# Performance work log

Hardware: AMD Instinct MI355X
Metric: run time of the kernel (lower is better)

Reference implementation:

```python
import jax, jax.numpy as jnp
import numpy as np

HIDDEN = 768
VOCAB = 32000
HS1 = 128


def setup_inputs() -> dict:
    key = jax.random.key(0)
    k_tk, k_hs, k_w1, k_b1, k_w2, k_b2 = jax.random.split(key, 6)
    B, S = 16, 4096
    tk = jax.random.randint(k_tk, (B, S), 0, VOCAB, dtype=jnp.int64)
    hs0 = jax.random.normal(k_hs, (B, S, HIDDEN), dtype=jnp.float32)
    # lin1: in_features = VOCAB + HIDDEN, out = HS1.  Stored as [in, out]
    # (transpose of torch's [out, in]); rows [0:VOCAB] multiply the one-hot,
    # rows [VOCAB:] multiply hs0, matching cat([one_hot, hs0], -1).
    bound1 = 1.0 / np.sqrt(VOCAB + HIDDEN)
    W1 = jax.random.uniform(k_w1, (VOCAB + HIDDEN, HS1), jnp.float32, -bound1, bound1)
    b1 = jax.random.uniform(k_b1, (HS1,), jnp.float32, -bound1, bound1)
    bound2 = 1.0 / np.sqrt(HS1)
    W2 = jax.random.uniform(k_w2, (HS1, 1), jnp.float32, -bound2, bound2)
    b2 = jax.random.uniform(k_b2, (1,), jnp.float32, -bound2, bound2)
    return {"tk": tk, "hs0": hs0, "W1": W1, "b1": b1, "W2": W2, "b2": b2}


def reference(tk, hs0, W1, b1, W2, b2):
    # one_hot(tk) @ W1[:VOCAB] is exactly a row gather (entries are 0/1),
    # so compute it as a gather fused with the hs0 projection.
    tok_part = W1[:VOCAB][tk]                      # [B, S, HS1] gather
    hs_part = jnp.einsum("bsh,hk->bsk", hs0, W1[VOCAB:])  # [B, S, HS1]
    h = jax.nn.relu(tok_part + hs_part + b1)       # [B, S, HS1]
    out = jnp.einsum("bsk,ko->bso", h, W2) + b2    # [B, S, 1]
    return out.squeeze(-1)                         # [B, S]
```

## Files before the change

### kernel.cpp

```cpp
#include <hip/hip_runtime.h>

#define HIDDEN 768
#define VOCAB  32000
#define HS1    128
#define KSTEPS (HIDDEN / 32)

typedef __attribute__((ext_vector_type(8))) short bf16x8;
typedef __attribute__((ext_vector_type(4))) float f32x4;

__device__ __forceinline__ unsigned short f2bf(float f) {
    union { float f; unsigned u; } x; x.f = f;
    unsigned r = x.u + 0x7fffu + ((x.u >> 16) & 1u);
    return (unsigned short)(r >> 16);
}

__global__ void pack_b_kernel(const float* __restrict__ W1,
                              unsigned short* __restrict__ Bp) {
    int idx  = blockIdx.x * 256 + threadIdx.x;
    int j    = idx & 7;
    int lane = (idx >> 3) & 63;
    int nt   = (idx >> 9) & 7;
    int ks   = idx >> 12;
    int k = ks * 32 + (lane >> 4) * 8 + j;
    int n = nt * 16 + (lane & 15);
    float v = W1[(size_t)(VOCAB + k) * HS1 + n];
    Bp[idx] = f2bf(v);
}

__launch_bounds__(256, 2)
__global__ void classifier_kernel(const int* __restrict__ tk,
                                  const float* __restrict__ hs0,
                                  const float* __restrict__ W1,
                                  const float* __restrict__ b1,
                                  const float* __restrict__ W2,
                                  const float* __restrict__ b2,
                                  const unsigned short* __restrict__ Bp,
                                  float* __restrict__ out) {
    const int lane = threadIdx.x & 63;
    const int wave = threadIdx.x >> 6;
    const int quad = lane >> 4;
    const int col  = lane & 15;
    const int row0 = (blockIdx.x * 4 + wave) * 32;

    const float* a0 = hs0 + (size_t)(row0 + col) * HIDDEN + quad * 8;
    const float* a1 = a0 + (size_t)16 * HIDDEN;
    const unsigned short* bp = Bp + lane * 8;

    f32x4 acc[2][8];
#pragma unroll
    for (int mt = 0; mt < 2; ++mt)
#pragma unroll
        for (int nt = 0; nt < 8; ++nt)
            acc[mt][nt] = (f32x4){0.f, 0.f, 0.f, 0.f};

    struct Frag {
        f32x4 a0l, a0h, a1l, a1h;
        bf16x8 b[8];
    };

    auto load_frag = [&](int ks) {
        Frag f;
        const float* pa0 = a0 + ks * 32;
        const float* pa1 = a1 + ks * 32;
        f.a0l = *(const f32x4*)(pa0);
        f.a0h = *(const f32x4*)(pa0 + 4);
        f.a1l = *(const f32x4*)(pa1);
        f.a1h = *(const f32x4*)(pa1 + 4);
        const unsigned short* pb = bp + ks * 4096;
#pragma unroll
        for (int nt = 0; nt < 8; ++nt)
            f.b[nt] = *(const bf16x8*)(pb + nt * 512);
        return f;
    };

    auto cvt8 = [&](f32x4 lo, f32x4 hi) {
        bf16x8 r;
        r[0] = (short)f2bf(lo[0]); r[1] = (short)f2bf(lo[1]);
        r[2] = (short)f2bf(lo[2]); r[3] = (short)f2bf(lo[3]);
        r[4] = (short)f2bf(hi[0]); r[5] = (short)f2bf(hi[1]);
        r[6] = (short)f2bf(hi[2]); r[7] = (short)f2bf(hi[3]);
        return r;
    };

    auto compute = [&](const Frag& f) {
        bf16x8 af0 = cvt8(f.a0l, f.a0h);
        bf16x8 af1 = cvt8(f.a1l, f.a1h);
#pragma unroll
        for (int nt = 0; nt < 8; ++nt) {
            acc[0][nt] = __builtin_amdgcn_mfma_f32_16x16x32_bf16(af0, f.b[nt], acc[0][nt], 0, 0, 0);
            acc[1][nt] = __builtin_amdgcn_mfma_f32_16x16x32_bf16(af1, f.b[nt], acc[1][nt], 0, 0, 0);
        }
    };

    Frag fa = load_frag(0);
    Frag fb = load_frag(1);
#pragma unroll 1
    for (int ks = 2; ks < KSTEPS; ks += 2) {
        compute(fa);
        fa = load_frag(ks);
        compute(fb);
        fb = load_frag(ks + 1);
    }
    compute(fa);
    compute(fb);

    const float bb2 = b2[0];
    float b1v[8], w2v[8];
#pragma unroll
    for (int nt = 0; nt < 8; ++nt) {
        b1v[nt] = b1[nt * 16 + col];
        w2v[nt] = W2[nt * 16 + col];
    }
#pragma unroll
    for (int mt = 0; mt < 2; ++mt) {
#pragma unroll
        for (int reg = 0; reg < 4; ++reg) {
            int r = row0 + mt * 16 + quad * 4 + reg;
            int token = tk[r];
            const float* wrow = W1 + (size_t)token * HS1;
            float p = 0.f;
#pragma unroll
            for (int nt = 0; nt < 8; ++nt) {
                float v = acc[mt][nt][reg] + wrow[nt * 16 + col] + b1v[nt];
                v = fmaxf(v, 0.f);
                p = fmaf(v, w2v[nt], p);
            }
            p += __shfl_xor(p, 1);
            p += __shfl_xor(p, 2);
            p += __shfl_xor(p, 4);
            p += __shfl_xor(p, 8);
            if (col == 0) out[r] = p + bb2;
        }
    }
}

extern "C" void kernel_launch(void* const* d_in, const int* in_sizes, int n_in,
                              void* d_out, int out_size, void* d_ws, size_t ws_size,
                              hipStream_t stream) {
    const int*   tk  = (const int*)d_in[0];
    const float* hs0 = (const float*)d_in[1];
    const float* W1  = (const float*)d_in[2];
    const float* b1  = (const float*)d_in[3];
    const float* W2  = (const float*)d_in[4];
    const float* b2  = (const float*)d_in[5];
    float* out = (float*)d_out;
    unsigned short* Bp = (unsigned short*)d_ws;

    pack_b_kernel<<<(HIDDEN * HS1) / 256, 256, 0, stream>>>(W1, Bp);

    int n_tokens = in_sizes[0];
    int grid = n_tokens / 128;
    classifier_kernel<<<grid, 256, 0, stream>>>(tk, hs0, W1, b1, W2, b2, Bp, out);
}
```

Measured before the change: 311.8 us.

## Deepen hs0 prefetch to three stages, use nontemporal loads, hoist token reads

The main K loop now keeps three fragments in flight instead of two, so more of the streaming hs0 memory latency is hidden behind MFMA work. The hs0 loads become nontemporal so the streamed activations do not evict the packed weights from cache. Token ids are read before the GEMM loop so the gather addresses are ready at the epilogue. The extra fragment raises register use, which under launch_bounds(256,2) may cause spills or lower occupancy.

```diff
diff --git a/kernel.cpp b/kernel.cpp
--- a/kernel.cpp
+++ b/kernel.cpp
@@ -42,9 +42,16 @@
     const int col  = lane & 15;
     const int row0 = (blockIdx.x * 4 + wave) * 32;
 
-    const float* a0 = hs0 + (size_t)(row0 + col) * HIDDEN + quad * 8;
-    const float* a1 = a0 + (size_t)16 * HIDDEN;
-    const unsigned short* bp = Bp + lane * 8;
+    const float* pa0 = hs0 + (size_t)(row0 + col) * HIDDEN + quad * 8;
+    const float* pa1 = pa0 + (size_t)16 * HIDDEN;
+    const unsigned short* pb0 = Bp + lane * 8;
+
+    int toks[8];
+#pragma unroll
+    for (int mt = 0; mt < 2; ++mt)
+#pragma unroll
+        for (int reg = 0; reg < 4; ++reg)
+            toks[mt * 4 + reg] = tk[row0 + mt * 16 + quad * 4 + reg];
 
     f32x4 acc[2][8];
 #pragma unroll
@@ -60,16 +67,19 @@
 
     auto load_frag = [&](int ks) {
         Frag f;
-        const float* pa0 = a0 + ks * 32;
-        const float* pa1 = a1 + ks * 32;
-        f.a0l = *(const f32x4*)(pa0);
-        f.a0h = *(const f32x4*)(pa0 + 4);
-        f.a1l = *(const f32x4*)(pa1);
-        f.a1h = *(const f32x4*)(pa1 + 4);
-        const unsigned short* pb = bp + ks * 4096;
+        const f32x4* x0 = (const f32x4*)(pa0 + ks * 32);
+        const f32x4* x1 = (const f32x4*)(pa1 + ks * 32);
+        f.a0l = __builtin_nontemporal_load(x0);
+        f.a0h = __builtin_nontemporal_load(x0 + 1);
+        f.a1l = __builtin_nontemporal_load(x1);
+        f.a1h = __builtin_nontemporal_load(x1 + 1);
+        const unsigned short* pb  = pb0 + ks * 4096;
+        const unsigned short* pb2 = pb + 2048;
 #pragma unroll
-        for (int nt = 0; nt < 8; ++nt)
-            f.b[nt] = *(const bf16x8*)(pb + nt * 512);
+        for (int nt = 0; nt < 4; ++nt) {
+            f.b[nt]     = *(const bf16x8*)(pb  + nt * 512);
+            f.b[nt + 4] = *(const bf16x8*)(pb2 + nt * 512);
+        }
         return f;
     };
 
@@ -92,17 +102,18 @@
         }
     };
 
-    Frag fa = load_frag(0);
-    Frag fb = load_frag(1);
+    Frag f0 = load_frag(0);
+    Frag f1 = load_frag(1);
+    Frag f2 = load_frag(2);
 #pragma unroll 1
-    for (int ks = 2; ks < KSTEPS; ks += 2) {
-        compute(fa);
-        fa = load_frag(ks);
-        compute(fb);
-        fb = load_frag(ks + 1);
+    for (int ks = 3; ks < KSTEPS; ks += 3) {
+        compute(f0); f0 = load_frag(ks);
+        compute(f1); f1 = load_frag(ks + 1);
+        compute(f2); f2 = load_frag(ks + 2);
     }
-    compute(fa);
-    compute(fb);
+    compute(f0);
+    compute(f1);
+    compute(f2);
 
     const float bb2 = b2[0];
     float b1v[8], w2v[8];
@@ -116,8 +127,7 @@
 #pragma unroll
         for (int reg = 0; reg < 4; ++reg) {
             int r = row0 + mt * 16 + quad * 4 + reg;
-            int token = tk[r];
-            const float* wrow = W1 + (size_t)token * HS1;
+            const float* wrow = W1 + (size_t)toks[mt * 4 + reg] * HS1;
             float p = 0.f;
 #pragma unroll
             for (int nt = 0; nt < 8; ++nt) {
```

Result: faster. 304.4 us (-2.4%).
